# Performance work log

Measured on AMD Instinct MI355X. Metric: run time of the kernel, lower is better.

Reference implementation:

```python
import jax, jax.numpy as jnp
import numpy as np
from jax import lax

B, N, C, T = 32, 1000, 32, 24
K, F_CHEB, F_TIME = 3, 64, 64


def setup_inputs() -> dict:
    key = jax.random.key(0)
    ks = jax.random.split(key, 7)
    return {
        "x": jax.random.normal(ks[0], (B, N, C, T), dtype=jnp.float32),
        "cheb_T": jax.random.normal(ks[1], (K, N, N), dtype=jnp.float32) * (1.0 / np.sqrt(N)),
        "Theta": jax.random.normal(ks[2], (K, C, F_CHEB), dtype=jnp.float32) * 0.1,
        "time_w": jax.random.normal(ks[3], (F_TIME, F_CHEB, 1, 3), dtype=jnp.float32) * 0.05,
        "time_b": jax.random.normal(ks[4], (F_TIME,), dtype=jnp.float32) * 0.05,
        "res_w": jax.random.normal(ks[5], (F_TIME, C, 1, 1), dtype=jnp.float32) * 0.1,
        "res_b": jax.random.normal(ks[6], (F_TIME,), dtype=jnp.float32) * 0.05,
    }


def _conv2d(x, w, stride_t, pad_t):
    # x: [B, Cin, N, T] (NCHW with H=nodes, W=time), w: [Cout, Cin, kh, kw]
    return lax.conv_general_dilated(
        x, w, window_strides=(1, stride_t), padding=((0, 0), (pad_t, pad_t)),
        dimension_numbers=("NCHW", "OIHW", "NCHW"))


def reference(x, cheb_T, Theta, time_w, time_b, res_w, res_b):
    # ChebConv: rhs_k[b,n,c,t] = sum_m T_k[m,n] x[b,m,c,t]; out = sum_k rhs_k @ Theta_k
    # Fused over all timesteps and polynomial orders in one einsum.
    spatial = jax.nn.relu(
        jnp.einsum("knm,bmct,kcf->bnft", cheb_T, x, Theta))  # [B,N,F_cheb,T]
    # time conv over the T axis (kernel (1,3), pad (0,1), stride (1,1))
    h = spatial.transpose(0, 2, 1, 3)  # [B,F_cheb,N,T]
    tc = _conv2d(h, time_w, 1, 1) + time_b[None, :, None, None]
    tc = jnp.tanh(tc) * jax.nn.sigmoid(tc)  # wave-net gating
    # 1x1 residual conv on the raw input (Dropout output in source is unused)
    res = _conv2d(x.transpose(0, 2, 1, 3), res_w, 1, 0) + res_b[None, :, None, None]
    out = (res + tc).transpose(0, 2, 1, 3)  # [B,N,F_time,T]
    return out
```

## Files before the change

### kernel.cpp

```cpp
#include <hip/hip_runtime.h>
#include <math.h>

typedef __attribute__((ext_vector_type(4))) float f32x4;
typedef __attribute__((ext_vector_type(8))) short s16x8;
typedef __attribute__((ext_vector_type(8))) unsigned short u16x8;
typedef __attribute__((ext_vector_type(4))) unsigned short u16x4;

#define NB 32
#define NN 1000
#define NT 24
#define NP 1024
#define TCN 768

#define GLOAD16(g, l) __builtin_amdgcn_global_load_lds( \
    (const __attribute__((address_space(1))) unsigned int*)(g), \
    (__attribute__((address_space(3))) unsigned int*)(l), 16, 0, 0)

__device__ __forceinline__ unsigned short f2bf(float f){
  union { float fv; unsigned int u; } v; v.fv = f;
  unsigned int r = v.u + 0x7FFFu + ((v.u >> 16) & 1u);
  return (unsigned short)(r >> 16);
}

__global__ void k0_cheb(const float* __restrict__ cheb, unsigned short* __restrict__ cbT){
  int idx = blockIdx.x * 256 + threadIdx.x;
  int base = idx << 2;
  int m = base & (NP - 1);
  int r = base >> 10;
  int n = r & (NP - 1);
  int k = r >> 10;
  u16x4 o;
  #pragma unroll
  for (int i = 0; i < 4; ++i){
    int mm = m + i;
    float v = (n < NN && mm < NN) ? cheb[((long)k*NN + n)*NN + mm] : 0.f;
    o[i] = f2bf(v);
  }
  *(u16x4*)(cbT + base) = o;
}

__global__ __launch_bounds__(256) void k0_x(const float* __restrict__ x,
                     unsigned short* __restrict__ xbT, unsigned short* __restrict__ xt2){
  __shared__ unsigned short tile[64*770];
  const int b  = blockIdx.x >> 4;
  const int m0 = (blockIdx.x & 15) << 6;
  const int tid = threadIdx.x;
  for (int i = tid; i < 64*192; i += 256){
    int mi = i / 192, c4 = (i - mi*192) << 2;
    f32x4 v = (f32x4){0.f,0.f,0.f,0.f};
    if (m0 + mi < NN) v = *(const f32x4*)(x + (size_t)(b*NN + m0 + mi)*768 + c4);
    unsigned short* tp = tile + mi*770 + c4;
    tp[0] = f2bf(v[0]); tp[1] = f2bf(v[1]); tp[2] = f2bf(v[2]); tp[3] = f2bf(v[3]);
  }
  __syncthreads();
  {
    const int seg = tid & 7, r0 = tid >> 3;
    for (int rr = 0; rr < 768; rr += 32){
      int r = rr + r0;
      int t = r >> 5, c = r & 31, ct = c*24 + t;
      u16x8 v;
      #pragma unroll
      for (int e = 0; e < 8; ++e) v[e] = tile[(seg*8 + e)*770 + ct];
      *(u16x8*)(xbT + ((size_t)b*TCN + r)*NP + m0 + seg*8) = v;
    }
  }
  if (m0 < NN){
    int rows = NN - m0; if (rows > 64) rows = 64;
    for (int i = tid; i < rows*96; i += 256){
      int mi = i / 96, s = i - mi*96;
      u16x8 v;
      #pragma unroll
      for (int e = 0; e < 8; ++e){
        int r = s*8 + e; int t = r >> 5, c = r & 31;
        v[e] = tile[mi*770 + c*24 + t];
      }
      *(u16x8*)(xt2 + (size_t)(b*NN + m0 + mi)*TCN + s*8) = v;
    }
  }
}

__global__ void k0_w(const float* __restrict__ Theta, const float* __restrict__ tw,
                     const float* __restrict__ rw,
                     unsigned short* __restrict__ ThT, unsigned short* __restrict__ WtT,
                     unsigned short* __restrict__ rwT){
  int i = blockIdx.x * 256 + threadIdx.x;
  if (i < 64*96){
    int f = i / 96, kc = i - f*96;
    ThT[i] = f2bf(Theta[kc*64 + f]);
  }
  if (i < 64*192){
    int f = i / 192, kk = i - f*192;
    int dt = kk >> 6, fi = kk & 63;
    WtT[i] = f2bf(tw[(f*64 + fi)*3 + dt]);
  }
  if (i < 64*32){
    rwT[i] = f2bf(rw[i]);
  }
}

__global__ __launch_bounds__(256, 2) void k1_cheb_theta(
    const unsigned short* __restrict__ cbT,
    const unsigned short* __restrict__ xbT,
    const unsigned short* __restrict__ ThT,
    unsigned short* __restrict__ spa)
{
  __shared__ __align__(16) unsigned short smem[28672];

  int p = blockIdx.x;
  int lb = (p & 7) * 384 + (p >> 3);
  const int tct = lb % 12; lb /= 12;
  const int nt  = lb & 7;
  const int b   = lb >> 3;

  const int tid  = threadIdx.x;
  const int wid  = tid >> 6;
  const int lane = tid & 63;
  const int l16  = lane & 15;
  const int k8   = lane >> 4;

  const int rl  = lane >> 3;
  const int cg8 = (((lane & 7) ^ rl) << 3);

  const unsigned short* gA = cbT + (size_t)(nt*128 + rl) * NP + cg8;
  const unsigned short* gB = xbT + ((size_t)b*TCN + tct*64 + rl) * NP + cg8;

  f32x4 acc[3][2][4];
  #pragma unroll
  for (int k = 0; k < 3; ++k)
    #pragma unroll
    for (int i = 0; i < 2; ++i)
      #pragma unroll
      for (int j = 0; j < 4; ++j) acc[k][i][j] = (f32x4){0.f, 0.f, 0.f, 0.f};

  for (int step = 0; step < 16; ++step){
    __syncthreads();
    const int so = step * 64;
    #pragma unroll
    for (int q = 0; q < 14; ++q){
      const int g = wid * 14 + q;
      if (g < 48){
        const int k = g >> 4, row8 = g & 15;
        GLOAD16(gA + (size_t)k*NP*NP + (size_t)row8*8*NP + so,
                (char*)smem + k*16384 + row8*1024);
      } else {
        const int row8 = g - 48;
        GLOAD16(gB + (size_t)row8*8*NP + so,
                (char*)smem + 49152 + row8*1024);
      }
    }
    __syncthreads();
    #pragma unroll
    for (int ks = 0; ks < 2; ++ks){
      const int ph = (((ks << 2) + k8) ^ (l16 & 7)) << 3;
      s16x8 af[3][2], bf[4];
      #pragma unroll
      for (int k = 0; k < 3; ++k)
        #pragma unroll
        for (int i = 0; i < 2; ++i){
          const int ra = wid*32 + i*16 + l16;
          af[k][i] = *(const s16x8*)(smem + k*8192 + ra*64 + ph);
        }
      #pragma unroll
      for (int j = 0; j < 4; ++j){
        const int rb = j*16 + l16;
        bf[j] = *(const s16x8*)(smem + 24576 + rb*64 + ph);
      }
      #pragma unroll
      for (int k = 0; k < 3; ++k)
        #pragma unroll
        for (int i = 0; i < 2; ++i)
          #pragma unroll
          for (int j = 0; j < 4; ++j)
            acc[k][i][j] = __builtin_amdgcn_mfma_f32_16x16x32_bf16(af[k][i], bf[j], acc[k][i][j], 0, 0, 0);
    }
  }

  __syncthreads();
  unsigned short* yl = smem;
  #pragma unroll
  for (int k = 0; k < 3; ++k)
    #pragma unroll
    for (int i = 0; i < 2; ++i)
      #pragma unroll
      for (int j = 0; j < 4; ++j){
        const int t = j >> 1;
        const int c = ((j & 1) << 4) + l16;
        const int nb = wid*32 + i*16 + (k8 << 2);
        #pragma unroll
        for (int r = 0; r < 4; ++r)
          yl[(t*128 + nb + r)*104 + k*32 + c] = f2bf(acc[k][i][j][r]);
      }
  __syncthreads();

  s16x8 b2[3][4];
  #pragma unroll
  for (int ch = 0; ch < 3; ++ch)
    #pragma unroll
    for (int j = 0; j < 4; ++j)
      b2[ch][j] = *(const s16x8*)(ThT + (j*16 + l16)*96 + ch*32 + k8*8);

  f32x4 acc2[2][2][4];
  #pragma unroll
  for (int t = 0; t < 2; ++t)
    #pragma unroll
    for (int i = 0; i < 2; ++i)
      #pragma unroll
      for (int j = 0; j < 4; ++j) acc2[t][i][j] = (f32x4){0.f,0.f,0.f,0.f};

  #pragma unroll
  for (int t = 0; t < 2; ++t)
    #pragma unroll
    for (int i = 0; i < 2; ++i)
      #pragma unroll
      for (int ch = 0; ch < 3; ++ch){
        s16x8 a2 = *(const s16x8*)(yl + (size_t)(t*128 + wid*32 + i*16 + l16)*104 + ch*32 + k8*8);
        #pragma unroll
        for (int j = 0; j < 4; ++j)
          acc2[t][i][j] = __builtin_amdgcn_mfma_f32_16x16x32_bf16(a2, b2[ch][j], acc2[t][i][j], 0, 0, 0);
      }

  #pragma unroll
  for (int t = 0; t < 2; ++t)
    #pragma unroll
    for (int i = 0; i < 2; ++i)
      #pragma unroll
      for (int j = 0; j < 4; ++j)
        #pragma unroll
        for (int r = 0; r < 4; ++r){
          const int n = nt*128 + wid*32 + i*16 + (k8 << 2) + r;
          if (n < NN){
            const int f  = j*16 + l16;
            const int tg = tct*2 + t;
            spa[((size_t)(b*NN + n)*NT + tg)*64 + f] = f2bf(fmaxf(acc2[t][i][j][r], 0.f));
          }
        }
}

__global__ __launch_bounds__(256, 2) void k2_out(
    const unsigned short* __restrict__ spa, const unsigned short* __restrict__ xt2,
    const unsigned short* __restrict__ WtT, const unsigned short* __restrict__ rwT,
    const float* __restrict__ tb, const float* __restrict__ rb,
    float* __restrict__ out)
{
  const int tid  = threadIdx.x;
  const int wid  = tid >> 6;
  const int lane = tid & 63;
  const int l16  = lane & 15;
  const int k8   = lane >> 4;
  const int gwave = blockIdx.x * 4 + wid;

  s16x8 bw[6][4], br[4];
  #pragma unroll
  for (int ch = 0; ch < 6; ++ch)
    #pragma unroll
    for (int j = 0; j < 4; ++j)
      bw[ch][j] = *(const s16x8*)(WtT + (j*16 + l16)*192 + ch*32 + k8*8);
  #pragma unroll
  for (int j = 0; j < 4; ++j)
    br[j] = *(const s16x8*)(rwT + (j*16 + l16)*32 + k8*8);
  float tbv[4], rbv[4];
  #pragma unroll
  for (int j = 0; j < 4; ++j){ tbv[j] = tb[j*16 + l16]; rbv[j] = rb[j*16 + l16]; }

  for (int it = 0; it < 8; ++it){
    const int r0 = (gwave*8 + it) * 16;
    const int rowA = r0 + l16;
    const int tA = rowA % 24;
    const int bn = rowA / 24;
    f32x4 acc_tc[4], acc_res[4];
    #pragma unroll
    for (int j = 0; j < 4; ++j){ acc_tc[j] = (f32x4){0.f,0.f,0.f,0.f}; acc_res[j] = (f32x4){0.f,0.f,0.f,0.f}; }

    #pragma unroll
    for (int ch = 0; ch < 6; ++ch){
      const int dt = ch >> 1, fh = (ch & 1) << 5;
      const int ts = tA + dt - 1;
      s16x8 a = (s16x8){0,0,0,0,0,0,0,0};
      if (ts >= 0 && ts < 24)
        a = *(const s16x8*)(spa + ((size_t)(bn*24 + ts) << 6) + fh + k8*8);
      #pragma unroll
      for (int j = 0; j < 4; ++j)
        acc_tc[j] = __builtin_amdgcn_mfma_f32_16x16x32_bf16(a, bw[ch][j], acc_tc[j], 0, 0, 0);
    }
    {
      s16x8 a = *(const s16x8*)(xt2 + (size_t)bn*768 + tA*32 + k8*8);
      #pragma unroll
      for (int j = 0; j < 4; ++j)
        acc_res[j] = __builtin_amdgcn_mfma_f32_16x16x32_bf16(a, br[j], acc_res[j], 0, 0, 0);
    }

    const int rowD = r0 + (k8 << 2);
    const int tD  = rowD % 24;
    const int bnD = rowD / 24;
    #pragma unroll
    for (int j = 0; j < 4; ++j){
      f32x4 v;
      #pragma unroll
      for (int r = 0; r < 4; ++r){
        float z  = acc_tc[j][r] + tbv[j];
        float s  = 1.f / (1.f + __expf(-z));
        float th = 2.f / (1.f + __expf(-2.f*z)) - 1.f;
        v[r] = acc_res[j][r] + rbv[j] + th * s;
      }
      *(f32x4*)(out + (((size_t)bnD << 6) + j*16 + l16)*24 + tD) = v;
    }
  }
}

extern "C" void kernel_launch(void* const* d_in, const int* in_sizes, int n_in,
                              void* d_out, int out_size, void* d_ws, size_t ws_size,
                              hipStream_t stream) {
  const float* x     = (const float*)d_in[0];
  const float* cheb  = (const float*)d_in[1];
  const float* Theta = (const float*)d_in[2];
  const float* tw    = (const float*)d_in[3];
  const float* tb    = (const float*)d_in[4];
  const float* rw    = (const float*)d_in[5];
  const float* rb    = (const float*)d_in[6];
  float* out = (float*)d_out;

  char* ws = (char*)d_ws;
  size_t off = 0;
  auto alloc = [&](size_t bytes) -> void* {
    void* p = ws + off;
    off += (bytes + 255) & ~(size_t)255;
    return p;
  };
  unsigned short* cbT = (unsigned short*)alloc((size_t)3*NP*NP*2);
  unsigned short* xbT = (unsigned short*)alloc((size_t)NB*TCN*NP*2);
  unsigned short* xt2 = (unsigned short*)alloc((size_t)NB*NN*TCN*2);
  unsigned short* spa = (unsigned short*)alloc((size_t)NB*NN*NT*64*2);
  unsigned short* ThT = (unsigned short*)alloc((size_t)64*96*2);
  unsigned short* WtT = (unsigned short*)alloc((size_t)64*192*2);
  unsigned short* rwT = (unsigned short*)alloc((size_t)64*32*2);

  hipLaunchKernelGGL(k0_cheb, dim3(3072), dim3(256), 0, stream, cheb, cbT);
  hipLaunchKernelGGL(k0_x,    dim3(512),  dim3(256), 0, stream, x, xbT, xt2);
  hipLaunchKernelGGL(k0_w,    dim3(48),   dim3(256), 0, stream, Theta, tw, rw, ThT, WtT, rwT);
  hipLaunchKernelGGL(k1_cheb_theta, dim3(32*8*12), dim3(256), 0, stream, cbT, xbT, ThT, spa);
  hipLaunchKernelGGL(k2_out,  dim3(1500), dim3(256), 0, stream, spa, xt2, WtT, rwT, tb, rb, out);
}
```

Measured before the change: 443.9 us.

## Split Chebyshev GEMM across 8 waves with smaller K-tiles and fuse gating math

The Chebyshev-times-x GEMM kernel goes from 4 waves to 8 per block, arranged as a 4x2 wave grid. The K-tile shrinks from 64 to 32 with a new LDS swizzle, halving shared memory and the per-wave accumulator count so more blocks and waves can be resident. The Theta epilogue now runs in two passes over the timesteps to reuse the smaller LDS buffer. Separately, the tanh*sigmoid gating is rewritten in closed form as (1-e)/(1+e^2) with e = exp(-z), using one exp and a hardware reciprocal. This adds more barriers per K step and slightly lower precision in the gate.

```diff
diff --git a/kernel.cpp b/kernel.cpp
--- a/kernel.cpp
+++ b/kernel.cpp
@@ -98,16 +98,16 @@
   }
 }
 
-__global__ __launch_bounds__(256, 2) void k1_cheb_theta(
+__global__ __launch_bounds__(512, 4) void k1_cheb_theta(
     const unsigned short* __restrict__ cbT,
     const unsigned short* __restrict__ xbT,
     const unsigned short* __restrict__ ThT,
     unsigned short* __restrict__ spa)
 {
-  __shared__ __align__(16) unsigned short smem[28672];
-
-  int p = blockIdx.x;
-  int lb = (p & 7) * 384 + (p >> 3);
+  __shared__ __align__(16) unsigned short smem[14336];
+
+  int pB = blockIdx.x;
+  int lb = (pB & 7) * 384 + (pB >> 3);
   const int tct = lb % 12; lb /= 12;
   const int nt  = lb & 7;
   const int b   = lb >> 3;
@@ -117,123 +117,104 @@
   const int lane = tid & 63;
   const int l16  = lane & 15;
   const int k8   = lane >> 4;
-
-  const int rl  = lane >> 3;
-  const int cg8 = (((lane & 7) ^ rl) << 3);
-
-  const unsigned short* gA = cbT + (size_t)(nt*128 + rl) * NP + cg8;
-  const unsigned short* gB = xbT + ((size_t)b*TCN + tct*64 + rl) * NP + cg8;
-
-  f32x4 acc[3][2][4];
+  const int wr   = wid & 3;
+  const int wc   = wid >> 2;
+
+  const int rl4  = lane >> 2;
+  const int swz8 = (((lane & 3) ^ ((rl4 >> 1) & 3)) << 3);
+  const unsigned short* gA = cbT + (size_t)(nt*128 + rl4)*NP + swz8;
+  const unsigned short* gB = xbT + ((size_t)b*TCN + tct*64 + rl4)*NP + swz8;
+
+  const int rdsw = ((k8 ^ ((l16 >> 1) & 3)) << 3);
+
+  f32x4 acc[3][2][2];
   #pragma unroll
   for (int k = 0; k < 3; ++k)
     #pragma unroll
     for (int i = 0; i < 2; ++i)
       #pragma unroll
-      for (int j = 0; j < 4; ++j) acc[k][i][j] = (f32x4){0.f, 0.f, 0.f, 0.f};
-
-  for (int step = 0; step < 16; ++step){
+      for (int j = 0; j < 2; ++j) acc[k][i][j] = (f32x4){0.f, 0.f, 0.f, 0.f};
+
+  for (int step = 0; step < 32; ++step){
     __syncthreads();
-    const int so = step * 64;
-    #pragma unroll
-    for (int q = 0; q < 14; ++q){
-      const int g = wid * 14 + q;
-      if (g < 48){
-        const int k = g >> 4, row8 = g & 15;
-        GLOAD16(gA + (size_t)k*NP*NP + (size_t)row8*8*NP + so,
-                (char*)smem + k*16384 + row8*1024);
-      } else {
-        const int row8 = g - 48;
-        GLOAD16(gB + (size_t)row8*8*NP + so,
-                (char*)smem + 49152 + row8*1024);
+    const int so = step << 5;
+    #pragma unroll
+    for (int q = 0; q < 4; ++q){
+      const int g = wid + (q << 3);
+      if (g < 24){
+        const int k = g >> 3, rg = g & 7;
+        GLOAD16(gA + (size_t)k*NP*NP + (size_t)rg*16*NP + so,
+                (char*)smem + k*8192 + rg*1024);
+      } else if (g < 28){
+        const int rg = g - 24;
+        GLOAD16(gB + (size_t)rg*16*NP + so,
+                (char*)smem + 24576 + rg*1024);
       }
     }
     __syncthreads();
-    #pragma unroll
-    for (int ks = 0; ks < 2; ++ks){
-      const int ph = (((ks << 2) + k8) ^ (l16 & 7)) << 3;
-      s16x8 af[3][2], bf[4];
-      #pragma unroll
-      for (int k = 0; k < 3; ++k)
+    s16x8 af[3][2], bf[2];
+    #pragma unroll
+    for (int k = 0; k < 3; ++k)
+      #pragma unroll
+      for (int i = 0; i < 2; ++i)
+        af[k][i] = *(const s16x8*)(smem + k*4096 + (wr*32 + i*16 + l16)*32 + rdsw);
+    #pragma unroll
+    for (int j = 0; j < 2; ++j)
+      bf[j] = *(const s16x8*)(smem + 12288 + (wc*32 + j*16 + l16)*32 + rdsw);
+    #pragma unroll
+    for (int k = 0; k < 3; ++k)
+      #pragma unroll
+      for (int i = 0; i < 2; ++i)
         #pragma unroll
-        for (int i = 0; i < 2; ++i){
-          const int ra = wid*32 + i*16 + l16;
-          af[k][i] = *(const s16x8*)(smem + k*8192 + ra*64 + ph);
-        }
-      #pragma unroll
-      for (int j = 0; j < 4; ++j){
-        const int rb = j*16 + l16;
-        bf[j] = *(const s16x8*)(smem + 24576 + rb*64 + ph);
-      }
+        for (int j = 0; j < 2; ++j)
+          acc[k][i][j] = __builtin_amdgcn_mfma_f32_16x16x32_bf16(af[k][i], bf[j], acc[k][i][j], 0, 0, 0);
+  }
+
+  s16x8 b2[3][4];
+  #pragma unroll
+  for (int ch = 0; ch < 3; ++ch)
+    #pragma unroll
+    for (int j = 0; j < 4; ++j)
+      b2[ch][j] = *(const s16x8*)(ThT + (j*16 + l16)*96 + ch*32 + k8*8);
+
+  unsigned short* yl = smem;
+  #pragma unroll
+  for (int p = 0; p < 2; ++p){
+    __syncthreads();
+    if (wc == p){
       #pragma unroll
       for (int k = 0; k < 3; ++k)
         #pragma unroll
         for (int i = 0; i < 2; ++i)
           #pragma unroll
-          for (int j = 0; j < 4; ++j)
-            acc[k][i][j] = __builtin_amdgcn_mfma_f32_16x16x32_bf16(af[k][i], bf[j], acc[k][i][j], 0, 0, 0);
-    }
-  }
-
-  __syncthreads();
-  unsigned short* yl = smem;
-  #pragma unroll
-  for (int k = 0; k < 3; ++k)
-    #pragma unroll
-    for (int i = 0; i < 2; ++i)
-      #pragma unroll
-      for (int j = 0; j < 4; ++j){
-        const int t = j >> 1;
-        const int c = ((j & 1) << 4) + l16;
-        const int nb = wid*32 + i*16 + (k8 << 2);
-        #pragma unroll
-        for (int r = 0; r < 4; ++r)
-          yl[(t*128 + nb + r)*104 + k*32 + c] = f2bf(acc[k][i][j][r]);
+          for (int j = 0; j < 2; ++j){
+            const int nb = wr*32 + i*16 + (k8 << 2);
+            #pragma unroll
+            for (int r = 0; r < 4; ++r)
+              yl[(nb + r)*104 + k*32 + j*16 + l16] = f2bf(acc[k][i][j][r]);
+          }
+    }
+    __syncthreads();
+    f32x4 acc2[4];
+    #pragma unroll
+    for (int j = 0; j < 4; ++j) acc2[j] = (f32x4){0.f,0.f,0.f,0.f};
+    #pragma unroll
+    for (int ch = 0; ch < 3; ++ch){
+      s16x8 a2 = *(const s16x8*)(yl + (size_t)(wid*16 + l16)*104 + ch*32 + k8*8);
+      #pragma unroll
+      for (int j = 0; j < 4; ++j)
+        acc2[j] = __builtin_amdgcn_mfma_f32_16x16x32_bf16(a2, b2[ch][j], acc2[j], 0, 0, 0);
+    }
+    const int tg = tct*2 + p;
+    #pragma unroll
+    for (int j = 0; j < 4; ++j)
+      #pragma unroll
+      for (int r = 0; r < 4; ++r){
+        const int n = nt*128 + wid*16 + (k8 << 2) + r;
+        if (n < NN)
+          spa[((size_t)(b*NN + n)*NT + tg)*64 + j*16 + l16] = f2bf(fmaxf(acc2[j][r], 0.f));
       }
-  __syncthreads();
-
-  s16x8 b2[3][4];
-  #pragma unroll
-  for (int ch = 0; ch < 3; ++ch)
-    #pragma unroll
-    for (int j = 0; j < 4; ++j)
-      b2[ch][j] = *(const s16x8*)(ThT + (j*16 + l16)*96 + ch*32 + k8*8);
-
-  f32x4 acc2[2][2][4];
-  #pragma unroll
-  for (int t = 0; t < 2; ++t)
-    #pragma unroll
-    for (int i = 0; i < 2; ++i)
-      #pragma unroll
-      for (int j = 0; j < 4; ++j) acc2[t][i][j] = (f32x4){0.f,0.f,0.f,0.f};
-
-  #pragma unroll
-  for (int t = 0; t < 2; ++t)
-    #pragma unroll
-    for (int i = 0; i < 2; ++i)
-      #pragma unroll
-      for (int ch = 0; ch < 3; ++ch){
-        s16x8 a2 = *(const s16x8*)(yl + (size_t)(t*128 + wid*32 + i*16 + l16)*104 + ch*32 + k8*8);
-        #pragma unroll
-        for (int j = 0; j < 4; ++j)
-          acc2[t][i][j] = __builtin_amdgcn_mfma_f32_16x16x32_bf16(a2, b2[ch][j], acc2[t][i][j], 0, 0, 0);
-      }
-
-  #pragma unroll
-  for (int t = 0; t < 2; ++t)
-    #pragma unroll
-    for (int i = 0; i < 2; ++i)
-      #pragma unroll
-      for (int j = 0; j < 4; ++j)
-        #pragma unroll
-        for (int r = 0; r < 4; ++r){
-          const int n = nt*128 + wid*32 + i*16 + (k8 << 2) + r;
-          if (n < NN){
-            const int f  = j*16 + l16;
-            const int tg = tct*2 + t;
-            spa[((size_t)(b*NN + n)*NT + tg)*64 + f] = f2bf(fmaxf(acc2[t][i][j][r], 0.f));
-          }
-        }
+  }
 }
 
 __global__ __launch_bounds__(256, 2) void k2_out(
@@ -297,10 +278,10 @@
       f32x4 v;
       #pragma unroll
       for (int r = 0; r < 4; ++r){
-        float z  = acc_tc[j][r] + tbv[j];
-        float s  = 1.f / (1.f + __expf(-z));
-        float th = 2.f / (1.f + __expf(-2.f*z)) - 1.f;
-        v[r] = acc_res[j][r] + rbv[j] + th * s;
+        float z = acc_tc[j][r] + tbv[j];
+        float e = __expf(-z);
+        float p = (1.f - e) * __builtin_amdgcn_rcpf(1.f + e*e);
+        v[r] = acc_res[j][r] + rbv[j] + p;
       }
       *(f32x4*)(out + (((size_t)bnD << 6) + j*16 + l16)*24 + tD) = v;
     }
@@ -337,6 +318,6 @@
   hipLaunchKernelGGL(k0_cheb, dim3(3072), dim3(256), 0, stream, cheb, cbT);
   hipLaunchKernelGGL(k0_x,    dim3(512),  dim3(256), 0, stream, x, xbT, xt2);
   hipLaunchKernelGGL(k0_w,    dim3(48),   dim3(256), 0, stream, Theta, tw, rw, ThT, WtT, rwT);
-  hipLaunchKernelGGL(k1_cheb_theta, dim3(32*8*12), dim3(256), 0, stream, cbT, xbT, ThT, spa);
+  hipLaunchKernelGGL(k1_cheb_theta, dim3(32*8*12), dim3(512), 0, stream, cbT, xbT, ThT, spa);
   hipLaunchKernelGGL(k2_out,  dim3(1500), dim3(256), 0, stream, spa, xt2, WtT, rwT, tb, rb, out);
 }
```

Measured after the change: 457.5 us. 3.1% more time.
